# Performance work log

Hardware: AMD Instinct MI355X
Metric: run time of the kernel (lower is better)

The kernel has to match this reference:

```python
import jax, jax.numpy as jnp
import numpy as np

N = 100000
E = 1600000
IN, HID, OUT, HEADS = 256, 16, 64, 8
NEG_SLOPE = 0.2


def gat_conv(x, src, dst, W, att_s, att_d, bias, heads, out_c, concat):
    n = x.shape[0]
    h = (x @ W).reshape(n, heads, out_c)              # [N,H,C]
    a_s = jnp.einsum('nhc,hc->nh', h, att_s)          # [N,H]
    a_d = jnp.einsum('nhc,hc->nh', h, att_d)          # [N,H]
    logits = jax.nn.leaky_relu(a_s[src] + a_d[dst], NEG_SLOPE)  # [E,H]
    m = jax.ops.segment_max(logits, dst, num_segments=n)        # [N,H]
    m = jnp.where(jnp.isfinite(m), m, 0.0)
    e = jnp.exp(logits - m[dst])                                 # [E,H]
    denom = jax.ops.segment_sum(e, dst, num_segments=n)         # [N,H]
    alpha = e / (denom[dst] + 1e-16)                             # [E,H]
    msg = h[src] * alpha[:, :, None]                             # [E,H,C]
    out = jax.ops.segment_sum(msg, dst, num_segments=n)          # [N,H,C]
    out = out.reshape(n, heads * out_c) if concat else out.mean(axis=1)
    return out + bias


def setup_inputs() -> dict:
    key = jax.random.key(0)
    ks = jax.random.split(key, 10)
    g = lambda k, shp, fan: jax.random.normal(k, shp, jnp.float32) * np.sqrt(2.0 / fan)
    x = jax.random.normal(ks[0], (N, IN), jnp.float32)
    edge_index = jax.random.randint(ks[1], (2, E), 0, N, jnp.int32)
    W1 = g(ks[2], (IN, HEADS * HID), IN)
    att1_s = g(ks[3], (HEADS, HID), HID)
    att1_d = g(ks[4], (HEADS, HID), HID)
    b1 = jnp.zeros((HEADS * HID,), jnp.float32)
    W2 = g(ks[5], (HEADS * HID, OUT), HEADS * HID)
    att2_s = g(ks[6], (1, OUT), OUT)
    att2_d = g(ks[7], (1, OUT), OUT)
    b2 = jnp.zeros((OUT,), jnp.float32)
    return {"x": x, "edge_index": edge_index, "W1": W1, "att1_s": att1_s,
            "att1_d": att1_d, "b1": b1, "W2": W2, "att2_s": att2_s,
            "att2_d": att2_d, "b2": b2}


def reference(x, edge_index, W1, att1_s, att1_d, b1, W2, att2_s, att2_d, b2):
    src, dst = edge_index[0], edge_index[1]
    h = gat_conv(x, src, dst, W1, att1_s, att1_d, b1, HEADS, HID, True)
    h = jax.nn.elu(h)  # dropout = identity in eval mode
    h = gat_conv(h, src, dst, W2, att2_s, att2_d, b2, 1, OUT, False)
    return jax.nn.log_softmax(h, axis=1)
```

## Files before the change

### kernel.cpp

```cpp
#include <hip/hip_runtime.h>
#include <math.h>

#define N_NODES 100000
#define N_EDGES 1600000
#define GEMM1_BLOCKS ((N_NODES + 63) / 64)
#define FUSED_BLOCKS (GEMM1_BLOCKS * 5)

typedef __attribute__((ext_vector_type(8))) short short8;
typedef __attribute__((ext_vector_type(4))) float floatx4;

__device__ __forceinline__ float lrelu(float v) {
    return (v > 0.f) ? v : 0.2f * v;
}

__device__ __forceinline__ unsigned short f2bf(float f) {
    unsigned int u = __float_as_uint(f);
    u += 0x7fff + ((u >> 16) & 1);
    return (unsigned short)(u >> 16);
}

__device__ __forceinline__ float bflo(unsigned int u) { return __uint_as_float(u << 16); }
__device__ __forceinline__ float bfhi(unsigned int u) { return __uint_as_float(u & 0xffff0000u); }

__global__ void prep_kernel(const float* __restrict__ W1, const float* __restrict__ W2,
                            unsigned short* __restrict__ w1b, unsigned short* __restrict__ w2b) {
    int idx = blockIdx.x * 256 + threadIdx.x;
    if (idx < 4096) {
        int lane = idx & 63;
        int ts = idx >> 6;
        int t = ts >> 3, ks = ts & 7;
        int quad = lane >> 4, l15 = lane & 15;
        int kbase = ks * 32 + quad * 8;
        unsigned short o[8];
        #pragma unroll
        for (int j = 0; j < 8; j++)
            o[j] = f2bf(W1[(size_t)(kbase + j) * 128 + t * 16 + l15]);
        uint4 pk;
        pk.x = o[0] | ((unsigned int)o[1] << 16);
        pk.y = o[2] | ((unsigned int)o[3] << 16);
        pk.z = o[4] | ((unsigned int)o[5] << 16);
        pk.w = o[6] | ((unsigned int)o[7] << 16);
        ((uint4*)w1b)[idx] = pk;
    } else if (idx < 4096 + 1024) {
        int idx2 = idx - 4096;
        int lane = idx2 & 63;
        int ts = idx2 >> 6;
        int t = ts >> 2, ks = ts & 3;
        int quad = lane >> 4, l15 = lane & 15;
        int kbase = ks * 32 + quad * 8;
        unsigned short o[8];
        #pragma unroll
        for (int j = 0; j < 8; j++)
            o[j] = f2bf(W2[(size_t)(kbase + j) * 64 + t * 16 + l15]);
        uint4 pk;
        pk.x = o[0] | ((unsigned int)o[1] << 16);
        pk.y = o[2] | ((unsigned int)o[3] << 16);
        pk.z = o[4] | ((unsigned int)o[5] << 16);
        pk.w = o[6] | ((unsigned int)o[7] << 16);
        ((uint4*)w2b)[idx2] = pk;
    }
}

__global__ void __launch_bounds__(256) gemm1_link_kernel(
        const float* __restrict__ x, const short8* __restrict__ w1b,
        const float* __restrict__ att_s, const float* __restrict__ att_d,
        unsigned short* __restrict__ h1b, float* __restrict__ a1s, float* __restrict__ a1d,
        const int* __restrict__ ei, int* __restrict__ head, int2* __restrict__ rec8) {
    const int bid = blockIdx.x;
    if (bid % 5 != 0) {
        int lid = bid - bid / 5 - 1;
        int e = lid * 256 + threadIdx.x;
        if (e < N_EDGES) {
            int s = ei[e];
            int d = ei[N_EDGES + e];
            int old = atomicExch(&head[d], e);
            rec8[e] = make_int2(old, s);
        }
        return;
    }
    const int gid = bid / 5;
    const int lane = threadIdx.x & 63;
    const int wv = threadIdx.x >> 6;
    const int quad = lane >> 4;
    const int l15 = lane & 15;
    const int M = N_NODES;

    const int rowA = gid * 64 + wv * 16 + l15;
    const bool rowAok = rowA < M;
    const float4* xrow4 = (const float4*)(x + (size_t)rowA * 256);

    floatx4 acc[8];
    #pragma unroll
    for (int t = 0; t < 8; t++) acc[t] = (floatx4){0.f, 0.f, 0.f, 0.f};

    #pragma unroll
    for (int ks = 0; ks < 8; ks++) {
        float4 p0, p1;
        if (rowAok) {
            p0 = xrow4[ks * 8 + quad * 2];
            p1 = xrow4[ks * 8 + quad * 2 + 1];
        } else {
            p0 = make_float4(0.f, 0.f, 0.f, 0.f);
            p1 = p0;
        }
        short8 af;
        af[0] = (short)f2bf(p0.x); af[1] = (short)f2bf(p0.y);
        af[2] = (short)f2bf(p0.z); af[3] = (short)f2bf(p0.w);
        af[4] = (short)f2bf(p1.x); af[5] = (short)f2bf(p1.y);
        af[6] = (short)f2bf(p1.z); af[7] = (short)f2bf(p1.w);
        #pragma unroll
        for (int t = 0; t < 8; t++) {
            short8 bf = w1b[(t * 8 + ks) * 64 + lane];
            acc[t] = __builtin_amdgcn_mfma_f32_16x16x32_bf16(af, bf, acc[t], 0, 0, 0);
        }
    }

    const int rowC0 = gid * 64 + wv * 16 + quad * 4;
    #pragma unroll
    for (int t = 0; t < 8; t++) {
        float asw = att_s[t * 16 + l15];
        float adw = att_d[t * 16 + l15];
        #pragma unroll
        for (int r = 0; r < 4; r++) {
            int grow = rowC0 + r;
            float c = acc[t][r];
            if (grow < M) h1b[(size_t)grow * 128 + t * 16 + l15] = f2bf(c);
            float ps = c * asw;
            float pd = c * adw;
            ps += __shfl_xor(ps, 1, 64); ps += __shfl_xor(ps, 2, 64);
            ps += __shfl_xor(ps, 4, 64); ps += __shfl_xor(ps, 8, 64);
            pd += __shfl_xor(pd, 1, 64); pd += __shfl_xor(pd, 2, 64);
            pd += __shfl_xor(pd, 4, 64); pd += __shfl_xor(pd, 8, 64);
            if (l15 == 0 && grow < M) { a1s[grow * 8 + t] = ps; a1d[grow * 8 + t] = pd; }
        }
    }
}

__global__ void count_alloc_kernel(const int* __restrict__ head, const int2* __restrict__ rec8,
                                   int* __restrict__ rowstart, int* __restrict__ deg,
                                   int* __restrict__ counter, int n) {
    int i = blockIdx.x * 256 + threadIdx.x;
    int lane = threadIdx.x & 63;
    int c = 0;
    if (i < n) {
        int e = head[i];
        while (e >= 0) {
            e = ((const int*)rec8)[(size_t)e * 2];
            c++;
        }
    }
    int d = c;
    int pre = d;
    #pragma unroll
    for (int off = 1; off < 64; off <<= 1) {
        int v = __shfl_up(pre, off, 64);
        if (lane >= off) pre += v;
    }
    int total = __shfl(pre, 63, 64);
    int base = 0;
    if (lane == 63) base = atomicAdd(counter, total);
    base = __shfl(base, 63, 64);
    if (i < n) {
        rowstart[i] = base + pre - d;
        deg[i] = d;
    }
}

__global__ void flatten_kernel(const int* __restrict__ head, const int2* __restrict__ rec8,
                               const int* __restrict__ rowstart, int* __restrict__ csr_src,
                               int n) {
    int node = blockIdx.x * 256 + threadIdx.x;
    if (node >= n) return;
    int e = head[node];
    int c = rowstart[node];
    while (e >= 0) {
        int2 r = rec8[e];
        csr_src[c++] = r.y;
        e = r.x;
    }
}

__global__ void __launch_bounds__(256) agg1_kernel(
        const unsigned short* __restrict__ h1b, const float* __restrict__ a1s,
        const float* __restrict__ a1d, const int* __restrict__ rowstart,
        const int* __restrict__ deg, const int* __restrict__ csr_src,
        const float* __restrict__ b1, unsigned int* __restrict__ h2b, int n) {
    const int lane = threadIdx.x & 63;
    const int node = blockIdx.x * 4 + (threadIdx.x >> 6);
    if (node >= n) return;
    const int h = lane >> 3;
    const int start = rowstart[node];
    const int d = deg[node];
    const float ad = a1d[node * 8 + h];
    float l = 0.f, acc0 = 0.f, acc1 = 0.f;
    int i = 0;
    for (; i + 4 <= d; i += 4) {
        int s0 = csr_src[start + i];
        int s1 = csr_src[start + i + 1];
        int s2 = csr_src[start + i + 2];
        int s3 = csr_src[start + i + 3];
        float as0 = a1s[s0 * 8 + h];
        float as1 = a1s[s1 * 8 + h];
        float as2 = a1s[s2 * 8 + h];
        float as3 = a1s[s3 * 8 + h];
        unsigned int u0 = *(const unsigned int*)(h1b + (size_t)s0 * 128 + lane * 2);
        unsigned int u1 = *(const unsigned int*)(h1b + (size_t)s1 * 128 + lane * 2);
        unsigned int u2 = *(const unsigned int*)(h1b + (size_t)s2 * 128 + lane * 2);
        unsigned int u3 = *(const unsigned int*)(h1b + (size_t)s3 * 128 + lane * 2);
        float e0 = __expf(lrelu(as0 + ad));
        float e1 = __expf(lrelu(as1 + ad));
        float e2 = __expf(lrelu(as2 + ad));
        float e3 = __expf(lrelu(as3 + ad));
        l += (e0 + e1) + (e2 + e3);
        acc0 += e0 * bflo(u0) + e1 * bflo(u1) + e2 * bflo(u2) + e3 * bflo(u3);
        acc1 += e0 * bfhi(u0) + e1 * bfhi(u1) + e2 * bfhi(u2) + e3 * bfhi(u3);
    }
    for (; i < d; i++) {
        int s0 = csr_src[start + i];
        float as0 = a1s[s0 * 8 + h];
        unsigned int u0 = *(const unsigned int*)(h1b + (size_t)s0 * 128 + lane * 2);
        float e0 = __expf(lrelu(as0 + ad));
        l += e0;
        acc0 += e0 * bflo(u0);
        acc1 += e0 * bfhi(u0);
    }
    float inv = 1.f / (l + 1e-16f);
    float v0 = acc0 * inv + b1[lane * 2];
    float v1 = acc1 * inv + b1[lane * 2 + 1];
    v0 = (v0 > 0.f) ? v0 : expm1f(v0);
    v1 = (v1 > 0.f) ? v1 : expm1f(v1);
    h2b[(size_t)node * 64 + lane] = (unsigned int)f2bf(v0) | ((unsigned int)f2bf(v1) << 16);
}

__global__ void __launch_bounds__(256) gemm2_kernel(
        const short8* __restrict__ h2f, const short8* __restrict__ w2b,
        const float* __restrict__ att_s, const float* __restrict__ att_d,
        unsigned short* __restrict__ t2b, float* __restrict__ a2s, float* __restrict__ a2d,
        int n) {
    const int lane = threadIdx.x & 63;
    const int wv = threadIdx.x >> 6;
    const int quad = lane >> 4;
    const int l15 = lane & 15;

    const int rowA = blockIdx.x * 64 + wv * 16 + l15;
    const bool rowAok = rowA < n;

    floatx4 acc[4];
    #pragma unroll
    for (int t = 0; t < 4; t++) acc[t] = (floatx4){0.f, 0.f, 0.f, 0.f};

    #pragma unroll
    for (int ks = 0; ks < 4; ks++) {
        short8 af = {0, 0, 0, 0, 0, 0, 0, 0};
        if (rowAok) af = h2f[(size_t)rowA * 16 + ks * 4 + quad];
        #pragma unroll
        for (int t = 0; t < 4; t++) {
            short8 bf = w2b[(t * 4 + ks) * 64 + lane];
            acc[t] = __builtin_amdgcn_mfma_f32_16x16x32_bf16(af, bf, acc[t], 0, 0, 0);
        }
    }

    const int rowC0 = blockIdx.x * 64 + wv * 16 + quad * 4;
    float asw[4], adw[4];
    #pragma unroll
    for (int t = 0; t < 4; t++) {
        asw[t] = att_s[t * 16 + l15];
        adw[t] = att_d[t * 16 + l15];
    }
    #pragma unroll
    for (int r = 0; r < 4; r++) {
        int grow = rowC0 + r;
        bool ok = grow < n;
        float ps = 0.f, pd = 0.f;
        #pragma unroll
        for (int t = 0; t < 4; t++) {
            float c = acc[t][r];
            if (ok) t2b[(size_t)grow * 64 + t * 16 + l15] = f2bf(c);
            ps += c * asw[t];
            pd += c * adw[t];
        }
        ps += __shfl_xor(ps, 1, 64); ps += __shfl_xor(ps, 2, 64);
        ps += __shfl_xor(ps, 4, 64); ps += __shfl_xor(ps, 8, 64);
        pd += __shfl_xor(pd, 1, 64); pd += __shfl_xor(pd, 2, 64);
        pd += __shfl_xor(pd, 4, 64); pd += __shfl_xor(pd, 8, 64);
        if (l15 == 0 && ok) { a2s[grow] = ps; a2d[grow] = pd; }
    }
}

__global__ void __launch_bounds__(256) agg2_kernel(
        const unsigned short* __restrict__ t2b, const float* __restrict__ a2s,
        const float* __restrict__ a2d, const int* __restrict__ rowstart,
        const int* __restrict__ deg, const int* __restrict__ csr_src,
        const float* __restrict__ b2, float* __restrict__ out, int n) {
    const int lane = threadIdx.x & 63;
    const int node = blockIdx.x * 4 + (threadIdx.x >> 6);
    if (node >= n) return;
    const int start = rowstart[node];
    const int d = deg[node];
    const float ad = a2d[node];
    float l = 0.f, acc = 0.f;
    int i = 0;
    for (; i + 4 <= d; i += 4) {
        int s0 = csr_src[start + i];
        int s1 = csr_src[start + i + 1];
        int s2 = csr_src[start + i + 2];
        int s3 = csr_src[start + i + 3];
        float as0 = a2s[s0];
        float as1 = a2s[s1];
        float as2 = a2s[s2];
        float as3 = a2s[s3];
        unsigned short u0 = t2b[(size_t)s0 * 64 + lane];
        unsigned short u1 = t2b[(size_t)s1 * 64 + lane];
        unsigned short u2 = t2b[(size_t)s2 * 64 + lane];
        unsigned short u3 = t2b[(size_t)s3 * 64 + lane];
        float e0 = __expf(lrelu(as0 + ad));
        float e1 = __expf(lrelu(as1 + ad));
        float e2 = __expf(lrelu(as2 + ad));
        float e3 = __expf(lrelu(as3 + ad));
        l += (e0 + e1) + (e2 + e3);
        acc += e0 * __uint_as_float(((unsigned int)u0) << 16)
             + e1 * __uint_as_float(((unsigned int)u1) << 16)
             + e2 * __uint_as_float(((unsigned int)u2) << 16)
             + e3 * __uint_as_float(((unsigned int)u3) << 16);
    }
    for (; i < d; i++) {
        int s0 = csr_src[start + i];
        float as0 = a2s[s0];
        unsigned short u0 = t2b[(size_t)s0 * 64 + lane];
        float e0 = __expf(lrelu(as0 + ad));
        l += e0;
        acc += e0 * __uint_as_float(((unsigned int)u0) << 16);
    }
    float v = acc / (l + 1e-16f) + b2[lane];
    float mx = v;
    #pragma unroll
    for (int off = 32; off >= 1; off >>= 1) mx = fmaxf(mx, __shfl_xor(mx, off, 64));
    float ex = expf(v - mx);
    float s2 = ex;
    #pragma unroll
    for (int off = 32; off >= 1; off >>= 1) s2 += __shfl_xor(s2, off, 64);
    out[(size_t)node * 64 + lane] = v - mx - logf(s2);
}


extern "C" void kernel_launch(void* const* d_in, const int* in_sizes, int n_in,
                              void* d_out, int out_size, void* d_ws, size_t ws_size,
                              hipStream_t stream) {
    const float* x     = (const float*)d_in[0];
    const int*   ei    = (const int*)d_in[1];
    const float* W1    = (const float*)d_in[2];
    const float* att1s = (const float*)d_in[3];
    const float* att1d = (const float*)d_in[4];
    const float* b1    = (const float*)d_in[5];
    const float* W2    = (const float*)d_in[6];
    const float* att2s = (const float*)d_in[7];
    const float* att2d = (const float*)d_in[8];
    const float* b2    = (const float*)d_in[9];
    float* out = (float*)d_out;

    const int N = N_NODES, E = N_EDGES;

    char* p = (char*)d_ws;
    auto take = [&](size_t bytes) {
        char* r = p;
        p += (bytes + 255) & ~(size_t)255;
        return (void*)r;
    };
    int*            head     = (int*)take((size_t)N * 4);
    int*            deg      = (int*)take((size_t)N * 4);
    int*            rowstart = (int*)take((size_t)N * 4);
    int*            counter  = (int*)take(256);
    int2*           rec8     = (int2*)take((size_t)E * 8);
    int*            csr_src  = (int*)take((size_t)E * 4);
    unsigned short* w1b      = (unsigned short*)take(64 * 64 * 16);
    unsigned short* w2b      = (unsigned short*)take(16 * 64 * 16);
    unsigned short* h1b      = (unsigned short*)take((size_t)N * 128 * 2);
    float*          a1s      = (float*)take((size_t)N * 8 * 4);
    float*          a1d      = (float*)take((size_t)N * 8 * 4);
    unsigned int*   h2b      = (unsigned int*)take((size_t)N * 64 * 4);
    unsigned short* t2b      = (unsigned short*)take((size_t)N * 64 * 2);
    float* a2s = a1s;
    float* a2d = a1d;

    hipMemsetAsync(head, 0xFF, (size_t)N * 4, stream);
    hipMemsetAsync(counter, 0, 4, stream);

    prep_kernel<<<20, 256, 0, stream>>>(W1, W2, w1b, w2b);
    gemm1_link_kernel<<<FUSED_BLOCKS, 256, 0, stream>>>(
        x, (const short8*)w1b, att1s, att1d, h1b, a1s, a1d, ei, head, rec8);
    count_alloc_kernel<<<(N + 255) / 256, 256, 0, stream>>>(head, rec8, rowstart, deg,
                                                            counter, N);
    flatten_kernel<<<(N + 255) / 256, 256, 0, stream>>>(head, rec8, rowstart, csr_src, N);
    agg1_kernel<<<(N + 3) / 4, 256, 0, stream>>>(h1b, a1s, a1d, rowstart, deg, csr_src,
                                                 b1, h2b, N);
    gemm2_kernel<<<(N + 63) / 64, 256, 0, stream>>>((const short8*)h2b, (const short8*)w2b,
                                                    att2s, att2d, t2b, a2s, a2d, N);
    agg2_kernel<<<(N + 3) / 4, 256, 0, stream>>>(t2b, a2s, a2d, rowstart, deg, csr_src,
                                                 b2, out, N);
}
```

Baseline: 488.9 us.

## Build CSR via degree count, scan and atomic scatter instead of linked lists

Drops the per-destination linked-list construction (atomicExch heads plus pointer-chasing count and flatten kernels). The GEMM1 kernel now also counts in-degrees with atomicAdd on vectorised edge loads. A scan then computes row starts, and a scatter kernel places each source into the CSR with an atomic cursor. This removes the serial dependent-load chains per node and the 8-byte link records, at the cost of a second pass over the edge list and a nondeterministic edge order within each row.

```diff
diff --git a/kernel.cpp b/kernel.cpp
--- a/kernel.cpp
+++ b/kernel.cpp
@@ -4,7 +4,7 @@
 #define N_NODES 100000
 #define N_EDGES 1600000
 #define GEMM1_BLOCKS ((N_NODES + 63) / 64)
-#define FUSED_BLOCKS (GEMM1_BLOCKS * 5)
+#define EDGE4_BLOCKS ((N_EDGES / 4 + 255) / 256)
 
 typedef __attribute__((ext_vector_type(8))) short short8;
 typedef __attribute__((ext_vector_type(4))) float floatx4;
@@ -61,24 +61,25 @@
     }
 }
 
-__global__ void __launch_bounds__(256) gemm1_link_kernel(
+__global__ void __launch_bounds__(256) gemm1_deg_kernel(
         const float* __restrict__ x, const short8* __restrict__ w1b,
         const float* __restrict__ att_s, const float* __restrict__ att_d,
         unsigned short* __restrict__ h1b, float* __restrict__ a1s, float* __restrict__ a1d,
-        const int* __restrict__ ei, int* __restrict__ head, int2* __restrict__ rec8) {
+        const int* __restrict__ ei, int* __restrict__ deg) {
     const int bid = blockIdx.x;
-    if (bid % 5 != 0) {
-        int lid = bid - bid / 5 - 1;
-        int e = lid * 256 + threadIdx.x;
-        if (e < N_EDGES) {
-            int s = ei[e];
-            int d = ei[N_EDGES + e];
-            int old = atomicExch(&head[d], e);
-            rec8[e] = make_int2(old, s);
-        }
-        return;
-    }
-    const int gid = bid / 5;
+
+    {
+        int e4 = (bid * 256 + (int)threadIdx.x) * 4;
+        if (e4 < N_EDGES) {
+            const int4 dd = *(const int4*)(ei + N_EDGES + e4);
+            atomicAdd(&deg[dd.x], 1);
+            atomicAdd(&deg[dd.y], 1);
+            atomicAdd(&deg[dd.z], 1);
+            atomicAdd(&deg[dd.w], 1);
+        }
+    }
+
+    const int gid = bid;
     const int lane = threadIdx.x & 63;
     const int wv = threadIdx.x >> 6;
     const int quad = lane >> 4;
@@ -136,20 +137,11 @@
     }
 }
 
-__global__ void count_alloc_kernel(const int* __restrict__ head, const int2* __restrict__ rec8,
-                                   int* __restrict__ rowstart, int* __restrict__ deg,
-                                   int* __restrict__ counter, int n) {
+__global__ void scan_kernel(const int* __restrict__ deg, int* __restrict__ rowstart,
+                            int* __restrict__ cursor, int* __restrict__ counter, int n) {
     int i = blockIdx.x * 256 + threadIdx.x;
     int lane = threadIdx.x & 63;
-    int c = 0;
-    if (i < n) {
-        int e = head[i];
-        while (e >= 0) {
-            e = ((const int*)rec8)[(size_t)e * 2];
-            c++;
-        }
-    }
-    int d = c;
+    int d = (i < n) ? deg[i] : 0;
     int pre = d;
     #pragma unroll
     for (int off = 1; off < 64; off <<= 1) {
@@ -161,23 +153,26 @@
     if (lane == 63) base = atomicAdd(counter, total);
     base = __shfl(base, 63, 64);
     if (i < n) {
-        rowstart[i] = base + pre - d;
-        deg[i] = d;
-    }
-}
-
-__global__ void flatten_kernel(const int* __restrict__ head, const int2* __restrict__ rec8,
-                               const int* __restrict__ rowstart, int* __restrict__ csr_src,
-                               int n) {
-    int node = blockIdx.x * 256 + threadIdx.x;
-    if (node >= n) return;
-    int e = head[node];
-    int c = rowstart[node];
-    while (e >= 0) {
-        int2 r = rec8[e];
-        csr_src[c++] = r.y;
-        e = r.x;
-    }
+        int rs = base + pre - d;
+        rowstart[i] = rs;
+        cursor[i] = rs;
+    }
+}
+
+__global__ void scatter_kernel(const int* __restrict__ ei, int* __restrict__ cursor,
+                               int* __restrict__ csr_src) {
+    int e4 = (blockIdx.x * 256 + (int)threadIdx.x) * 4;
+    if (e4 >= N_EDGES) return;
+    int4 s = *(const int4*)(ei + e4);
+    int4 d = *(const int4*)(ei + N_EDGES + e4);
+    int p0 = atomicAdd(&cursor[d.x], 1);
+    int p1 = atomicAdd(&cursor[d.y], 1);
+    int p2 = atomicAdd(&cursor[d.z], 1);
+    int p3 = atomicAdd(&cursor[d.w], 1);
+    csr_src[p0] = s.x;
+    csr_src[p1] = s.y;
+    csr_src[p2] = s.z;
+    csr_src[p3] = s.w;
 }
 
 __global__ void __launch_bounds__(256) agg1_kernel(
@@ -366,11 +361,10 @@
         p += (bytes + 255) & ~(size_t)255;
         return (void*)r;
     };
-    int*            head     = (int*)take((size_t)N * 4);
     int*            deg      = (int*)take((size_t)N * 4);
     int*            rowstart = (int*)take((size_t)N * 4);
+    int*            cursor   = (int*)take((size_t)N * 4);
     int*            counter  = (int*)take(256);
-    int2*           rec8     = (int2*)take((size_t)E * 8);
     int*            csr_src  = (int*)take((size_t)E * 4);
     unsigned short* w1b      = (unsigned short*)take(64 * 64 * 16);
     unsigned short* w2b      = (unsigned short*)take(16 * 64 * 16);
@@ -382,15 +376,14 @@
     float* a2s = a1s;
     float* a2d = a1d;
 
-    hipMemsetAsync(head, 0xFF, (size_t)N * 4, stream);
+    hipMemsetAsync(deg, 0, (size_t)N * 4, stream);
     hipMemsetAsync(counter, 0, 4, stream);
 
     prep_kernel<<<20, 256, 0, stream>>>(W1, W2, w1b, w2b);
-    gemm1_link_kernel<<<FUSED_BLOCKS, 256, 0, stream>>>(
-        x, (const short8*)w1b, att1s, att1d, h1b, a1s, a1d, ei, head, rec8);
-    count_alloc_kernel<<<(N + 255) / 256, 256, 0, stream>>>(head, rec8, rowstart, deg,
-                                                            counter, N);
-    flatten_kernel<<<(N + 255) / 256, 256, 0, stream>>>(head, rec8, rowstart, csr_src, N);
+    gemm1_deg_kernel<<<GEMM1_BLOCKS, 256, 0, stream>>>(
+        x, (const short8*)w1b, att1s, att1d, h1b, a1s, a1d, ei, deg);
+    scan_kernel<<<(N + 255) / 256, 256, 0, stream>>>(deg, rowstart, cursor, counter, N);
+    scatter_kernel<<<EDGE4_BLOCKS, 256, 0, stream>>>(ei, cursor, csr_src);
     agg1_kernel<<<(N + 3) / 4, 256, 0, stream>>>(h1b, a1s, a1d, rowstart, deg, csr_src,
                                                  b1, h2b, N);
     gemm2_kernel<<<(N + 63) / 64, 256, 0, stream>>>((const short8*)h2b, (const short8*)w2b,
```

After: 585.3 us. +19.7%, slower.
